# Kernel tuning notes

Measured on AMD Instinct MI355X. Metric: run time of the kernel, lower is better.

Reference implementation:

```python
import jax, jax.numpy as jnp
import numpy as np
import math

D_MODEL = 1024
NUM_HEADS = 16
D_K = D_MODEL // NUM_HEADS
NUM_BUCKETS = 32
MAX_DISTANCE = 512  # PositionalEncoding max_len


def _relative_position_bucket(relative_position):
    # Faithful to the torch code: both signs add num_buckets//2 (==16), rp==0 adds 0.
    half = NUM_BUCKETS // 2            # 16
    max_exact = NUM_BUCKETS // 4       # 8
    base = (relative_position > 0).astype(jnp.int32) * half \
         + (relative_position < 0).astype(jnp.int32) * half
    arp = jnp.abs(relative_position)
    is_small = arp < max_exact
    safe = jnp.maximum(arp, 1).astype(jnp.float32)  # avoid log(0); masked by is_small anyway
    large = max_exact + (jnp.log(safe / max_exact)
                         / math.log(MAX_DISTANCE / max_exact)
                         * (half - max_exact)).astype(jnp.int32)  # trunc == torch .long()
    large = jnp.minimum(large, half - 1)
    return base + jnp.where(is_small, arp, large)


def compute_bias(rel_bias_table, seq_length):
    ctx = jnp.arange(seq_length, dtype=jnp.int32)[:, None]
    mem = jnp.arange(seq_length, dtype=jnp.int32)[None, :]
    buckets = _relative_position_bucket(mem - ctx)        # [S, S]
    values = rel_bias_table[buckets]                       # [S, S, H]
    return jnp.transpose(values, (2, 0, 1))[None]          # [1, H, S, S]


def setup_inputs() -> dict:
    key = jax.random.key(0)
    ks = jax.random.split(key, 12)
    B, S, D = 2, 2048, D_MODEL
    scale = 1.0 / math.sqrt(D)
    inp = {
        "query": jax.random.normal(ks[0], (B, S, D), jnp.float32),
        "key": jax.random.normal(ks[1], (B, S, D), jnp.float32),
        "value": jax.random.normal(ks[2], (B, S, D), jnp.float32),
        "Wq": jax.random.normal(ks[3], (D, D), jnp.float32) * scale,
        "bq": jnp.zeros((D,), jnp.float32),
        "Wk": jax.random.normal(ks[4], (D, D), jnp.float32) * scale,
        "bk": jnp.zeros((D,), jnp.float32),
        "Wv": jax.random.normal(ks[5], (D, D), jnp.float32) * scale,
        "bv": jnp.zeros((D,), jnp.float32),
        "Wo": jax.random.normal(ks[6], (D, D), jnp.float32) * scale,
        "bo": jnp.zeros((D,), jnp.float32),
        "rel_bias_table": jax.random.normal(ks[7], (NUM_BUCKETS, NUM_HEADS), jnp.float32) * 0.1,
    }
    return inp


def reference(query, key, value, Wq, bq, Wk, bk, Wv, bv, Wo, bo, rel_bias_table):
    B, Sq, D = query.shape
    Sk = key.shape[1]
    H, dk = NUM_HEADS, D_K
    q = (query @ Wq + bq).reshape(B, Sq, H, dk)
    k = (key @ Wk + bk).reshape(B, Sk, H, dk)
    v = (value @ Wv + bv).reshape(B, Sk, H, dk)
    scores = jnp.einsum('bqhd,bkhd->bhqk', q, k) / math.sqrt(dk)  # [B,H,Sq,Sk]
    position_bias = compute_bias(rel_bias_table, max(Sq, Sk))[:, :, :Sq, :Sk]
    scores = scores + position_bias  # broadcast over batch (torch expand)
    attn_weights = jax.nn.softmax(scores, axis=-1)
    # dropout is identity in eval / p=0
    context = jnp.einsum('bhqk,bkhd->bqhd', attn_weights, v).reshape(B, Sq, D)
    output = context @ Wo + bo
    pb = jnp.broadcast_to(position_bias, (B, H, Sq, Sk))
    return output, attn_weights, pb
```

## Files before the change

### kernel.cpp

```cpp
#include <hip/hip_runtime.h>
#include <hip/hip_bf16.h>

#define BN 2
#define SEQ 2048
#define DM 1024
#define NH 16
#define DK 64

using f32x4  = __attribute__((ext_vector_type(4))) float;
using bf16x8 = __attribute__((ext_vector_type(8))) __bf16;
using short8 = __attribute__((ext_vector_type(8))) short;

static_assert(sizeof(bf16x8) == 16, "bf16x8 must be 16B");

#define MFMA16(a, b, c) __builtin_amdgcn_mfma_f32_16x16x32_bf16(a, b, c, 0, 0, 0)

__device__ __forceinline__ unsigned short f2b(float f) {
    __hip_bfloat16 h = __float2bfloat16(f);
    return __builtin_bit_cast(unsigned short, h);
}

__device__ __forceinline__ bf16x8 load_bf8(const unsigned short* p) {
    short8 s = *reinterpret_cast<const short8*>(p);
    return __builtin_bit_cast(bf16x8, s);
}

__global__ void bias_table_kernel(const float* __restrict__ rel,
                                  float* __restrict__ bias_val) {
    int idx = blockIdx.x * 256 + threadIdx.x;
    if (idx >= NH * 4095) return;
    int h = idx / 4095;
    int dd = idx - h * 4095;
    int d = dd - 2047;
    int a = d < 0 ? -d : d;
    int bucket;
    if (a == 0) bucket = 0;
    else if (a < 8) bucket = 16 + a;
    else {
        int k = (a >= 14) + (a >= 23) + (a >= 39) + (a >= 64) +
                (a >= 108) + (a >= 182) + (a >= 305);
        bucket = 24 + k;
    }
    bias_val[h * 4095 + dd] = rel[bucket * NH + h];
}

__global__ __launch_bounds__(256) void wtrans_kernel(
        const float* __restrict__ W0, const float* __restrict__ W1,
        const float* __restrict__ W2, const float* __restrict__ W3,
        unsigned short* __restrict__ T0, unsigned short* __restrict__ T1,
        unsigned short* __restrict__ T2, unsigned short* __restrict__ T3) {
    constexpr int P = 68;
    __shared__ unsigned short lt[64 * P];
    const int mz = blockIdx.z;
    const float* W = mz == 0 ? W0 : mz == 1 ? W1 : mz == 2 ? W2 : W3;
    unsigned short* T = mz == 0 ? T0 : mz == 1 ? T1 : mz == 2 ? T2 : T3;
    const int k0 = blockIdx.x * 64, n0 = blockIdx.y * 64;
    const int tid = threadIdx.x;
#pragma unroll
    for (int p = 0; p < 4; ++p) {
        int r = p * 16 + (tid >> 4);
        int c = (tid & 15) * 4;
        float4 vv = *(const float4*)&W[(size_t)(k0 + r) * DM + n0 + c];
#pragma unroll
        for (int j = 0; j < 4; ++j) {
            int n = c + j;
            float x = j == 0 ? vv.x : j == 1 ? vv.y : j == 2 ? vv.z : vv.w;
            lt[n * P + (r ^ ((n & 7) << 3))] = f2b(x);
        }
    }
    __syncthreads();
#pragma unroll
    for (int p = 0; p < 2; ++p) {
        int rn = p * 32 + (tid >> 3);
        int ck = (tid & 7) * 8;
        int ckx = ck ^ ((rn & 7) << 3);
        ushort4 a0 = *(ushort4*)&lt[rn * P + ckx];
        ushort4 a1 = *(ushort4*)&lt[rn * P + ckx + 4];
        *(ushort4*)&T[(size_t)(n0 + rn) * DM + k0 + ck] = a0;
        *(ushort4*)&T[(size_t)(n0 + rn) * DM + k0 + ck + 4] = a1;
    }
}

__global__ __launch_bounds__(256) void qkv_gemm(
        const float* __restrict__ Aq, const float* __restrict__ Ak, const float* __restrict__ Av,
        const unsigned short* __restrict__ Wtq, const unsigned short* __restrict__ Wtk,
        const unsigned short* __restrict__ Wtv,
        const float* __restrict__ bq, const float* __restrict__ bk, const float* __restrict__ bv,
        unsigned short* __restrict__ Qp, unsigned short* __restrict__ Kh,
        unsigned short* __restrict__ Vt) {
    constexpr int KP = 40;
    __shared__ unsigned short la[128 * KP];
    __shared__ unsigned short lb[128 * KP];
    const int mat = blockIdx.z;
    const float* A = mat == 0 ? Aq : mat == 1 ? Ak : Av;
    const unsigned short* Wt = mat == 0 ? Wtq : mat == 1 ? Wtk : Wtv;
    const float* bias = mat == 0 ? bq : mat == 1 ? bk : bv;
    const float outscale = mat == 0 ? 0.125f : 1.0f;
    const int tid = threadIdx.x;
    const int m0 = blockIdx.y * 128, n0 = blockIdx.x * 128;
    const int lane = tid & 63, wid = tid >> 6;
    const int wm0 = (wid >> 1) * 64, wn0 = (wid & 1) * 64;
    const int l15 = lane & 15, l4 = lane >> 4;
    f32x4 acc[4][4] = {};

    for (int kt = 0; kt < 32; ++kt) {
        const int k0 = kt * 32;
#pragma unroll
        for (int i = 0; i < 4; ++i) {
            int idx = tid + i * 256;
            int row = idx >> 3, c4 = (idx & 7) * 4;
            float4 v = *(const float4*)(A + (size_t)(m0 + row) * DM + k0 + c4);
            ushort4 u; u.x = f2b(v.x); u.y = f2b(v.y); u.z = f2b(v.z); u.w = f2b(v.w);
            *(ushort4*)&la[row * KP + c4] = u;
        }
#pragma unroll
        for (int i = 0; i < 2; ++i) {
            int idx = tid + i * 256;
            int row = idx >> 2, c8 = (idx & 3) * 8;
            *(int4*)&lb[row * KP + c8] =
                *(const int4*)&Wt[(size_t)(n0 + row) * DM + k0 + c8];
        }
        __syncthreads();
        bf16x8 af[4], bfv[4];
#pragma unroll
        for (int m = 0; m < 4; ++m)
            af[m] = load_bf8(&la[(wm0 + m * 16 + l15) * KP + l4 * 8]);
#pragma unroll
        for (int n = 0; n < 4; ++n)
            bfv[n] = load_bf8(&lb[(wn0 + n * 16 + l15) * KP + l4 * 8]);
#pragma unroll
        for (int m = 0; m < 4; ++m)
#pragma unroll
            for (int n = 0; n < 4; ++n)
                acc[m][n] = MFMA16(af[m], bfv[n], acc[m][n]);
        __syncthreads();
    }

    float bv4[4];
#pragma unroll
    for (int n = 0; n < 4; ++n) bv4[n] = bias[n0 + wn0 + n * 16 + l15];
#pragma unroll
    for (int m = 0; m < 4; ++m) {
#pragma unroll
        for (int n = 0; n < 4; ++n) {
            int gcol = n0 + wn0 + n * 16 + l15;
#pragma unroll
            for (int r = 0; r < 4; ++r) {
                int grow = m0 + wm0 + m * 16 + l4 * 4 + r;
                float val = (acc[m][n][r] + bv4[n]) * outscale;
                unsigned short ob = f2b(val);
                int b = grow >> 11, s = grow & 2047;
                int hh = gcol >> 6, dl = gcol & 63;
                if (mat == 0) {
                    Qp[(size_t)grow * DM + gcol] = ob;
                } else if (mat == 1) {
                    Kh[(((size_t)(b * NH + hh) * SEQ + s) << 6) + dl] = ob;
                } else {
                    Vt[(((size_t)(b * NH + hh) * DK + dl) << 11) + s] = ob;
                }
            }
        }
    }
}

__global__ __launch_bounds__(256) void o_gemm(
        const unsigned short* __restrict__ Actx, const unsigned short* __restrict__ Wto,
        const float* __restrict__ bo, float* __restrict__ out) {
    constexpr int KP = 40;
    __shared__ unsigned short la[64 * KP];
    __shared__ unsigned short lb[128 * KP];
    const int tid = threadIdx.x;
    const int m0 = blockIdx.y * 64, n0 = blockIdx.x * 128;
    const int lane = tid & 63, wid = tid >> 6;
    const int wm0 = (wid >> 1) * 32, wn0 = (wid & 1) * 64;
    const int l15 = lane & 15, l4 = lane >> 4;
    f32x4 acc[2][4] = {};

    for (int kt = 0; kt < 32; ++kt) {
        const int k0 = kt * 32;
        {
            int row = tid >> 2, c8 = (tid & 3) * 8;
            *(int4*)&la[row * KP + c8] =
                *(const int4*)&Actx[(size_t)(m0 + row) * DM + k0 + c8];
        }
#pragma unroll
        for (int i = 0; i < 2; ++i) {
            int idx = tid + i * 256;
            int row = idx >> 2, c8 = (idx & 3) * 8;
            *(int4*)&lb[row * KP + c8] =
                *(const int4*)&Wto[(size_t)(n0 + row) * DM + k0 + c8];
        }
        __syncthreads();
        bf16x8 af[2], bfv[4];
#pragma unroll
        for (int m = 0; m < 2; ++m)
            af[m] = load_bf8(&la[(wm0 + m * 16 + l15) * KP + l4 * 8]);
#pragma unroll
        for (int n = 0; n < 4; ++n)
            bfv[n] = load_bf8(&lb[(wn0 + n * 16 + l15) * KP + l4 * 8]);
#pragma unroll
        for (int m = 0; m < 2; ++m)
#pragma unroll
            for (int n = 0; n < 4; ++n)
                acc[m][n] = MFMA16(af[m], bfv[n], acc[m][n]);
        __syncthreads();
    }

#pragma unroll
    for (int m = 0; m < 2; ++m)
#pragma unroll
        for (int n = 0; n < 4; ++n) {
            int gcol = n0 + wn0 + n * 16 + l15;
            float bb = bo[gcol];
#pragma unroll
            for (int r = 0; r < 4; ++r) {
                int grow = m0 + wm0 + m * 16 + l4 * 4 + r;
                out[(size_t)grow * DM + gcol] = acc[m][n][r] + bb;
            }
        }
}

__global__ __launch_bounds__(256, 4) void attn5_kernel(
        const unsigned short* __restrict__ Qp, const unsigned short* __restrict__ Kh,
        const unsigned short* __restrict__ Vt, const float* __restrict__ bias_val,
        float* __restrict__ attn_out, float* __restrict__ pb_out,
        unsigned short* __restrict__ ctx) {
    __shared__ float bias_lds[2112];
    __shared__ float wtile[2][4][16 * 36];
    const int tid = threadIdx.x;
    const int lane = tid & 63, wid = tid >> 6;
    const int l15 = lane & 15, l4 = lane >> 4;
    const int bid = (blockIdx.x & 7) * 128 + (blockIdx.x >> 3);
    const int qb = bid & 31;
    const int h = (bid >> 5) & 15;
    const int b = bid >> 9;
    const int q0 = qb * 64;
    const int qw = q0 + wid * 16;

    {
        const float* bp = bias_val + h * 4095 + (2047 - (q0 + 63));
        for (int i = tid; i < 2111; i += 256) bias_lds[i] = bp[i];
    }
    __syncthreads();

    const unsigned short* qbase = Qp + (size_t)(b * SEQ + qw + l15) * DM + h * DK;
    bf16x8 qa0 = load_bf8(qbase + l4 * 8);
    bf16x8 qa1 = load_bf8(qbase + 32 + l4 * 8);

    const unsigned short* kbase = Kh + (((size_t)(b * NH + h) * SEQ) << 6);
    const int bbase = 63 - wid * 16 - l4 * 4;

    float m[4], l[4];
#pragma unroll
    for (int r = 0; r < 4; ++r) { m[r] = -3e38f; l[r] = 0.f; }

    for (int c0 = 0; c0 < SEQ; c0 += 32) {
        const unsigned short* kp = kbase + ((size_t)(c0 + l15) << 6);
        bf16x8 k00 = load_bf8(kp + l4 * 8);
        bf16x8 k01 = load_bf8(kp + 32 + l4 * 8);
        bf16x8 k10 = load_bf8(kp + (16 << 6) + l4 * 8);
        bf16x8 k11 = load_bf8(kp + (16 << 6) + 32 + l4 * 8);
        f32x4 a0 = {}, a1 = {};
        a0 = MFMA16(qa0, k00, a0); a0 = MFMA16(qa1, k01, a0);
        a1 = MFMA16(qa0, k10, a1); a1 = MFMA16(qa1, k11, a1);
#pragma unroll
        for (int r = 0; r < 4; ++r) {
            float s0 = a0[r] + bias_lds[c0 + l15 + bbase - r];
            float s1 = a1[r] + bias_lds[c0 + 16 + l15 + bbase - r];
            float cm = fmaxf(s0, s1);
            if (cm > m[r]) { l[r] *= __expf(m[r] - cm); m[r] = cm; }
            l[r] += __expf(s0 - m[r]) + __expf(s1 - m[r]);
        }
    }
#pragma unroll
    for (int off = 1; off < 16; off <<= 1) {
#pragma unroll
        for (int r = 0; r < 4; ++r) {
            float om = __shfl_xor(m[r], off);
            float ol = __shfl_xor(l[r], off);
            float M = fmaxf(m[r], om);
            l[r] = l[r] * __expf(m[r] - M) + ol * __expf(om - M);
            m[r] = M;
        }
    }
    float invl[4];
#pragma unroll
    for (int r = 0; r < 4; ++r) invl[r] = 1.0f / l[r];

    float* abase = attn_out + ((size_t)((b * NH + h) * SEQ + qw)) * SEQ;
    float* pbase = pb_out + ((size_t)((b * NH + h) * SEQ + qw)) * SEQ;
    const unsigned short* vbase = Vt + (((size_t)(b * NH + h) * DK) << 11);
    f32x4 cacc[4] = {};

    bf16x8 k00, k01, k10, k11;
    {
        const unsigned short* kp = kbase + ((size_t)l15 << 6);
        k00 = load_bf8(kp + l4 * 8);
        k01 = load_bf8(kp + 32 + l4 * 8);
        k10 = load_bf8(kp + (16 << 6) + l4 * 8);
        k11 = load_bf8(kp + (16 << 6) + 32 + l4 * 8);
    }
    const int srow = lane >> 2, scg = (lane & 3) * 8;
    int cur = 0;
    for (int c0 = 0; c0 < SEQ; c0 += 32, cur ^= 1) {
        f32x4 a0 = {}, a1 = {};
        a0 = MFMA16(qa0, k00, a0); a0 = MFMA16(qa1, k01, a0);
        a1 = MFMA16(qa0, k10, a1); a1 = MFMA16(qa1, k11, a1);
        const int cn = (c0 + 32) & (SEQ - 1);
        const unsigned short* kp = kbase + ((size_t)(cn + l15) << 6);
        k00 = load_bf8(kp + l4 * 8);
        k01 = load_bf8(kp + 32 + l4 * 8);
        k10 = load_bf8(kp + (16 << 6) + l4 * 8);
        k11 = load_bf8(kp + (16 << 6) + 32 + l4 * 8);
        bf16x8 vv0 = load_bf8(vbase + ((size_t)(0 * 16 + l15) << 11) + c0 + l4 * 8);
        bf16x8 vv1 = load_bf8(vbase + ((size_t)(1 * 16 + l15) << 11) + c0 + l4 * 8);
        bf16x8 vv2 = load_bf8(vbase + ((size_t)(2 * 16 + l15) << 11) + c0 + l4 * 8);
        bf16x8 vv3 = load_bf8(vbase + ((size_t)(3 * 16 + l15) << 11) + c0 + l4 * 8);
        float* wt = wtile[cur][wid];
#pragma unroll
        for (int r = 0; r < 4; ++r) {
            int row = l4 * 4 + r;
            float w0 = __expf(a0[r] + bias_lds[c0 + l15 + bbase - r] - m[r]) * invl[r];
            float w1 = __expf(a1[r] + bias_lds[c0 + 16 + l15 + bbase - r] - m[r]) * invl[r];
            wt[row * 36 + l15] = w0;
            wt[row * 36 + 16 + l15] = w1;
        }
        asm volatile("s_waitcnt lgkmcnt(0)" ::: "memory");
        __builtin_amdgcn_sched_barrier(0);
        {
            float4 v0 = *(const float4*)&wt[srow * 36 + scg];
            float4 v1 = *(const float4*)&wt[srow * 36 + scg + 4];
            float* gp = abase + (size_t)srow * SEQ + c0 + scg;
            *(float4*)gp = v0;
            *(float4*)(gp + 4) = v1;
        }
        {
            const int ib = c0 + scg + bbase + l4 * 4 - srow;
            float4 p0, p1;
            p0.x = bias_lds[ib + 0]; p0.y = bias_lds[ib + 1];
            p0.z = bias_lds[ib + 2]; p0.w = bias_lds[ib + 3];
            p1.x = bias_lds[ib + 4]; p1.y = bias_lds[ib + 5];
            p1.z = bias_lds[ib + 6]; p1.w = bias_lds[ib + 7];
            float* gp = pbase + (size_t)srow * SEQ + c0 + scg;
            *(float4*)gp = p0;
            *(float4*)(gp + 4) = p1;
        }
        float4 pA = *(const float4*)&wt[l15 * 36 + l4 * 8];
        float4 pB = *(const float4*)&wt[l15 * 36 + l4 * 8 + 4];
        short8 ps;
        ps[0] = (short)f2b(pA.x); ps[1] = (short)f2b(pA.y);
        ps[2] = (short)f2b(pA.z); ps[3] = (short)f2b(pA.w);
        ps[4] = (short)f2b(pB.x); ps[5] = (short)f2b(pB.y);
        ps[6] = (short)f2b(pB.z); ps[7] = (short)f2b(pB.w);
        bf16x8 pf = __builtin_bit_cast(bf16x8, ps);
        cacc[0] = MFMA16(pf, vv0, cacc[0]);
        cacc[1] = MFMA16(pf, vv1, cacc[1]);
        cacc[2] = MFMA16(pf, vv2, cacc[2]);
        cacc[3] = MFMA16(pf, vv3, cacc[3]);
    }
#pragma unroll
    for (int d0 = 0; d0 < 4; ++d0)
#pragma unroll
        for (int r = 0; r < 4; ++r)
            ctx[(size_t)(b * SEQ + qw + l4 * 4 + r) * DM + h * DK + d0 * 16 + l15] =
                f2b(cacc[d0][r]);
}

extern "C" void kernel_launch(void* const* d_in, const int* in_sizes, int n_in,
                              void* d_out, int out_size, void* d_ws, size_t ws_size,
                              hipStream_t stream) {
    const float* query = (const float*)d_in[0];
    const float* key   = (const float*)d_in[1];
    const float* value = (const float*)d_in[2];
    const float* Wq = (const float*)d_in[3];
    const float* bq = (const float*)d_in[4];
    const float* Wk = (const float*)d_in[5];
    const float* bk = (const float*)d_in[6];
    const float* Wv = (const float*)d_in[7];
    const float* bv = (const float*)d_in[8];
    const float* Wo = (const float*)d_in[9];
    const float* bo = (const float*)d_in[10];
    const float* rel = (const float*)d_in[11];

    float* out = (float*)d_out;
    float* attn_out = out + (size_t)BN * SEQ * DM;
    float* pb_out = attn_out + (size_t)BN * NH * SEQ * SEQ;

    char* ws = (char*)d_ws;
    float* bias_val = (float*)ws;
    unsigned short* Qp  = (unsigned short*)(ws + 262144);
    unsigned short* Kh  = Qp + (size_t)BN * SEQ * DM;
    unsigned short* Vt  = Kh + (size_t)BN * SEQ * DM;
    unsigned short* ctx = Vt + (size_t)BN * SEQ * DM;
    unsigned short* Wtq = ctx + (size_t)BN * SEQ * DM;
    unsigned short* Wtk = Wtq + (size_t)DM * DM;
    unsigned short* Wtv = Wtk + (size_t)DM * DM;
    unsigned short* Wto = Wtv + (size_t)DM * DM;

    bias_table_kernel<<<256, 256, 0, stream>>>(rel, bias_val);
    wtrans_kernel<<<dim3(16, 16, 4), 256, 0, stream>>>(Wq, Wk, Wv, Wo, Wtq, Wtk, Wtv, Wto);
    qkv_gemm<<<dim3(8, 32, 3), 256, 0, stream>>>(query, key, value, Wtq, Wtk, Wtv,
                                                 bq, bk, bv, Qp, Kh, Vt);
    attn5_kernel<<<BN * NH * (SEQ / 64), 256, 0, stream>>>(Qp, Kh, Vt, bias_val,
                                                           attn_out, pb_out, ctx);
    o_gemm<<<dim3(8, 64), 256, 0, stream>>>(ctx, Wto, bo, out);
}
```

Measured before the change: 592.8 us.

## Replace online softmax max with Cauchy-Schwarz bound and log-sum-exp normalization

Result: slower. 647.2 us (+9.2%).

```diff
diff --git a/kernel.cpp b/kernel.cpp
--- a/kernel.cpp
+++ b/kernel.cpp
@@ -87,7 +87,8 @@
         const unsigned short* __restrict__ Wtv,
         const float* __restrict__ bq, const float* __restrict__ bk, const float* __restrict__ bv,
         unsigned short* __restrict__ Qp, unsigned short* __restrict__ Kh,
-        unsigned short* __restrict__ Vt) {
+        unsigned short* __restrict__ Vt,
+        float* __restrict__ qnorm, float* __restrict__ khpart) {
     constexpr int KP = 40;
     __shared__ unsigned short la[128 * KP];
     __shared__ unsigned short lb[128 * KP];
@@ -139,6 +140,12 @@
     float bv4[4];
 #pragma unroll
     for (int n = 0; n < 4; ++n) bv4[n] = bias[n0 + wn0 + n * 16 + l15];
+    float nsq[4][4];
+#pragma unroll
+    for (int m = 0; m < 4; ++m)
+#pragma unroll
+        for (int r = 0; r < 4; ++r) nsq[m][r] = 0.f;
+
 #pragma unroll
     for (int m = 0; m < 4; ++m) {
 #pragma unroll
@@ -148,6 +155,7 @@
             for (int r = 0; r < 4; ++r) {
                 int grow = m0 + wm0 + m * 16 + l4 * 4 + r;
                 float val = (acc[m][n][r] + bv4[n]) * outscale;
+                if (mat < 2) nsq[m][r] += val * val;
                 unsigned short ob = f2b(val);
                 int b = grow >> 11, s = grow & 2047;
                 int hh = gcol >> 6, dl = gcol & 63;
@@ -159,6 +167,43 @@
                     Vt[(((size_t)(b * NH + hh) * DK + dl) << 11) + s] = ob;
                 }
             }
+        }
+    }
+
+    if (mat < 2) {
+        const int hh = (n0 + wn0) >> 6;
+        const int bh = ((m0 + wm0) >> 11) * NH + hh;
+#pragma unroll
+        for (int m = 0; m < 4; ++m)
+#pragma unroll
+            for (int r = 0; r < 4; ++r) {
+                float s2 = nsq[m][r];
+                s2 += __shfl_xor(s2, 1);
+                s2 += __shfl_xor(s2, 2);
+                s2 += __shfl_xor(s2, 4);
+                s2 += __shfl_xor(s2, 8);
+                nsq[m][r] = s2;
+            }
+        if (mat == 0) {
+            if (l15 == 0) {
+#pragma unroll
+                for (int m = 0; m < 4; ++m)
+#pragma unroll
+                    for (int r = 0; r < 4; ++r) {
+                        int grow = m0 + wm0 + m * 16 + l4 * 4 + r;
+                        qnorm[bh * SEQ + (grow & 2047)] = sqrtf(nsq[m][r]);
+                    }
+            }
+        } else {
+            float rmax = 0.f;
+#pragma unroll
+            for (int m = 0; m < 4; ++m)
+#pragma unroll
+                for (int r = 0; r < 4; ++r) rmax = fmaxf(rmax, nsq[m][r]);
+            rmax = fmaxf(rmax, __shfl_xor(rmax, 16));
+            rmax = fmaxf(rmax, __shfl_xor(rmax, 32));
+            if (lane == 0)
+                khpart[bh * 32 + (((m0 + wm0) & 2047) >> 6)] = sqrtf(rmax);
         }
     }
 }
@@ -220,13 +265,15 @@
         }
 }
 
-__global__ __launch_bounds__(256, 4) void attn5_kernel(
+__global__ __launch_bounds__(256, 4) void attn6_kernel(
         const unsigned short* __restrict__ Qp, const unsigned short* __restrict__ Kh,
         const unsigned short* __restrict__ Vt, const float* __restrict__ bias_val,
+        const float* __restrict__ qnorm, const float* __restrict__ khpart,
         float* __restrict__ attn_out, float* __restrict__ pb_out,
         unsigned short* __restrict__ ctx) {
     __shared__ float bias_lds[2112];
     __shared__ float wtile[2][4][16 * 36];
+    __shared__ float redmax[4];
     const int tid = threadIdx.x;
     const int lane = tid & 63, wid = tid >> 6;
     const int l15 = lane & 15, l4 = lane >> 4;
@@ -236,62 +283,46 @@
     const int b = bid >> 9;
     const int q0 = qb * 64;
     const int qw = q0 + wid * 16;
-
+    const int bh = b * NH + h;
+
+    float pmax = -1e30f;
     {
         const float* bp = bias_val + h * 4095 + (2047 - (q0 + 63));
-        for (int i = tid; i < 2111; i += 256) bias_lds[i] = bp[i];
-    }
+        for (int i = tid; i < 2111; i += 256) {
+            float x = bp[i];
+            bias_lds[i] = x;
+            pmax = fmaxf(pmax, x);
+        }
+    }
+#pragma unroll
+    for (int off = 1; off < 64; off <<= 1) pmax = fmaxf(pmax, __shfl_xor(pmax, off));
+    if (lane == 0) redmax[wid] = pmax;
     __syncthreads();
+    const float bmax = fmaxf(fmaxf(redmax[0], redmax[1]), fmaxf(redmax[2], redmax[3]));
+
+    float khv = (lane < 32) ? khpart[bh * 32 + lane] : 0.f;
+#pragma unroll
+    for (int off = 1; off < 64; off <<= 1) khv = fmaxf(khv, __shfl_xor(khv, off));
+
+    float Mr[4];
+#pragma unroll
+    for (int r = 0; r < 4; ++r)
+        Mr[r] = qnorm[bh * SEQ + qw + l4 * 4 + r] * 1.01f * khv + bmax + 0.1f;
 
     const unsigned short* qbase = Qp + (size_t)(b * SEQ + qw + l15) * DM + h * DK;
     bf16x8 qa0 = load_bf8(qbase + l4 * 8);
     bf16x8 qa1 = load_bf8(qbase + 32 + l4 * 8);
 
-    const unsigned short* kbase = Kh + (((size_t)(b * NH + h) * SEQ) << 6);
+    const unsigned short* kbase = Kh + (((size_t)bh * SEQ) << 6);
+    const unsigned short* vbase = Vt + (((size_t)bh * DK) << 11);
     const int bbase = 63 - wid * 16 - l4 * 4;
-
-    float m[4], l[4];
-#pragma unroll
-    for (int r = 0; r < 4; ++r) { m[r] = -3e38f; l[r] = 0.f; }
-
-    for (int c0 = 0; c0 < SEQ; c0 += 32) {
-        const unsigned short* kp = kbase + ((size_t)(c0 + l15) << 6);
-        bf16x8 k00 = load_bf8(kp + l4 * 8);
-        bf16x8 k01 = load_bf8(kp + 32 + l4 * 8);
-        bf16x8 k10 = load_bf8(kp + (16 << 6) + l4 * 8);
-        bf16x8 k11 = load_bf8(kp + (16 << 6) + 32 + l4 * 8);
-        f32x4 a0 = {}, a1 = {};
-        a0 = MFMA16(qa0, k00, a0); a0 = MFMA16(qa1, k01, a0);
-        a1 = MFMA16(qa0, k10, a1); a1 = MFMA16(qa1, k11, a1);
-#pragma unroll
-        for (int r = 0; r < 4; ++r) {
-            float s0 = a0[r] + bias_lds[c0 + l15 + bbase - r];
-            float s1 = a1[r] + bias_lds[c0 + 16 + l15 + bbase - r];
-            float cm = fmaxf(s0, s1);
-            if (cm > m[r]) { l[r] *= __expf(m[r] - cm); m[r] = cm; }
-            l[r] += __expf(s0 - m[r]) + __expf(s1 - m[r]);
-        }
-    }
-#pragma unroll
-    for (int off = 1; off < 16; off <<= 1) {
-#pragma unroll
-        for (int r = 0; r < 4; ++r) {
-            float om = __shfl_xor(m[r], off);
-            float ol = __shfl_xor(l[r], off);
-            float M = fmaxf(m[r], om);
-            l[r] = l[r] * __expf(m[r] - M) + ol * __expf(om - M);
-            m[r] = M;
-        }
-    }
-    float invl[4];
-#pragma unroll
-    for (int r = 0; r < 4; ++r) invl[r] = 1.0f / l[r];
-
-    float* abase = attn_out + ((size_t)((b * NH + h) * SEQ + qw)) * SEQ;
-    float* pbase = pb_out + ((size_t)((b * NH + h) * SEQ + qw)) * SEQ;
-    const unsigned short* vbase = Vt + (((size_t)(b * NH + h) * DK) << 11);
-    f32x4 cacc[4] = {};
-
+    const int srow = lane >> 2, scg = (lane & 3) * 8;
+    const int bb2 = 63 - wid * 16;
+
+    float* pbase = pb_out + ((size_t)(bh * SEQ + qw)) * SEQ;
+    float* abase = attn_out + ((size_t)(bh * SEQ + qw)) * SEQ;
+
+    float lsum[4] = {0.f, 0.f, 0.f, 0.f};
     bf16x8 k00, k01, k10, k11;
     {
         const unsigned short* kp = kbase + ((size_t)l15 << 6);
@@ -300,9 +331,7 @@
         k10 = load_bf8(kp + (16 << 6) + l4 * 8);
         k11 = load_bf8(kp + (16 << 6) + 32 + l4 * 8);
     }
-    const int srow = lane >> 2, scg = (lane & 3) * 8;
-    int cur = 0;
-    for (int c0 = 0; c0 < SEQ; c0 += 32, cur ^= 1) {
+    for (int c0 = 0; c0 < SEQ; c0 += 32) {
         f32x4 a0 = {}, a1 = {};
         a0 = MFMA16(qa0, k00, a0); a0 = MFMA16(qa1, k01, a0);
         a1 = MFMA16(qa0, k10, a1); a1 = MFMA16(qa1, k11, a1);
@@ -312,16 +341,69 @@
         k01 = load_bf8(kp + 32 + l4 * 8);
         k10 = load_bf8(kp + (16 << 6) + l4 * 8);
         k11 = load_bf8(kp + (16 << 6) + 32 + l4 * 8);
-        bf16x8 vv0 = load_bf8(vbase + ((size_t)(0 * 16 + l15) << 11) + c0 + l4 * 8);
-        bf16x8 vv1 = load_bf8(vbase + ((size_t)(1 * 16 + l15) << 11) + c0 + l4 * 8);
-        bf16x8 vv2 = load_bf8(vbase + ((size_t)(2 * 16 + l15) << 11) + c0 + l4 * 8);
-        bf16x8 vv3 = load_bf8(vbase + ((size_t)(3 * 16 + l15) << 11) + c0 + l4 * 8);
+        {
+            const int ib = c0 + scg + bb2 - srow;
+            float4 p0, p1;
+            p0.x = bias_lds[ib + 0]; p0.y = bias_lds[ib + 1];
+            p0.z = bias_lds[ib + 2]; p0.w = bias_lds[ib + 3];
+            p1.x = bias_lds[ib + 4]; p1.y = bias_lds[ib + 5];
+            p1.z = bias_lds[ib + 6]; p1.w = bias_lds[ib + 7];
+            float* gp = pbase + (size_t)srow * SEQ + c0 + scg;
+            *(float4*)gp = p0;
+            *(float4*)(gp + 4) = p1;
+        }
+#pragma unroll
+        for (int r = 0; r < 4; ++r) {
+            float e0 = __expf(a0[r] + bias_lds[c0 + l15 + bbase - r] - Mr[r]);
+            float e1 = __expf(a1[r] + bias_lds[c0 + 16 + l15 + bbase - r] - Mr[r]);
+            lsum[r] += e0 + e1;
+        }
+    }
+    float Mlog[4];
+#pragma unroll
+    for (int r = 0; r < 4; ++r) {
+        float s = lsum[r];
+        s += __shfl_xor(s, 1);
+        s += __shfl_xor(s, 2);
+        s += __shfl_xor(s, 4);
+        s += __shfl_xor(s, 8);
+        Mlog[r] = Mr[r] + __logf(s);
+    }
+
+    f32x4 cacc[4] = {};
+    bf16x8 vv0, vv1, vv2, vv3;
+    {
+        const unsigned short* kp = kbase + ((size_t)l15 << 6);
+        k00 = load_bf8(kp + l4 * 8);
+        k01 = load_bf8(kp + 32 + l4 * 8);
+        k10 = load_bf8(kp + (16 << 6) + l4 * 8);
+        k11 = load_bf8(kp + (16 << 6) + 32 + l4 * 8);
+        vv0 = load_bf8(vbase + ((size_t)(0 * 16 + l15) << 11) + l4 * 8);
+        vv1 = load_bf8(vbase + ((size_t)(1 * 16 + l15) << 11) + l4 * 8);
+        vv2 = load_bf8(vbase + ((size_t)(2 * 16 + l15) << 11) + l4 * 8);
+        vv3 = load_bf8(vbase + ((size_t)(3 * 16 + l15) << 11) + l4 * 8);
+    }
+    int cur = 0;
+    for (int c0 = 0; c0 < SEQ; c0 += 32, cur ^= 1) {
+        f32x4 a0 = {}, a1 = {};
+        a0 = MFMA16(qa0, k00, a0); a0 = MFMA16(qa1, k01, a0);
+        a1 = MFMA16(qa0, k10, a1); a1 = MFMA16(qa1, k11, a1);
+        const int cn = (c0 + 32) & (SEQ - 1);
+        const unsigned short* kp = kbase + ((size_t)(cn + l15) << 6);
+        bf16x8 kn00 = load_bf8(kp + l4 * 8);
+        bf16x8 kn01 = load_bf8(kp + 32 + l4 * 8);
+        bf16x8 kn10 = load_bf8(kp + (16 << 6) + l4 * 8);
+        bf16x8 kn11 = load_bf8(kp + (16 << 6) + 32 + l4 * 8);
+        bf16x8 vn0 = load_bf8(vbase + ((size_t)(0 * 16 + l15) << 11) + cn + l4 * 8);
+        bf16x8 vn1 = load_bf8(vbase + ((size_t)(1 * 16 + l15) << 11) + cn + l4 * 8);
+        bf16x8 vn2 = load_bf8(vbase + ((size_t)(2 * 16 + l15) << 11) + cn + l4 * 8);
+        bf16x8 vn3 = load_bf8(vbase + ((size_t)(3 * 16 + l15) << 11) + cn + l4 * 8);
         float* wt = wtile[cur][wid];
 #pragma unroll
         for (int r = 0; r < 4; ++r) {
             int row = l4 * 4 + r;
-            float w0 = __expf(a0[r] + bias_lds[c0 + l15 + bbase - r] - m[r]) * invl[r];
-            float w1 = __expf(a1[r] + bias_lds[c0 + 16 + l15 + bbase - r] - m[r]) * invl[r];
+            float w0 = __expf(a0[r] + bias_lds[c0 + l15 + bbase - r] - Mlog[r]);
+            float w1 = __expf(a1[r] + bias_lds[c0 + 16 + l15 + bbase - r] - Mlog[r]);
             wt[row * 36 + l15] = w0;
             wt[row * 36 + 16 + l15] = w1;
         }
@@ -333,17 +415,6 @@
             float* gp = abase + (size_t)srow * SEQ + c0 + scg;
             *(float4*)gp = v0;
             *(float4*)(gp + 4) = v1;
-        }
-        {
-            const int ib = c0 + scg + bbase + l4 * 4 - srow;
-            float4 p0, p1;
-            p0.x = bias_lds[ib + 0]; p0.y = bias_lds[ib + 1];
-            p0.z = bias_lds[ib + 2]; p0.w = bias_lds[ib + 3];
-            p1.x = bias_lds[ib + 4]; p1.y = bias_lds[ib + 5];
-            p1.z = bias_lds[ib + 6]; p1.w = bias_lds[ib + 7];
-            float* gp = pbase + (size_t)srow * SEQ + c0 + scg;
-            *(float4*)gp = p0;
-            *(float4*)(gp + 4) = p1;
         }
         float4 pA = *(const float4*)&wt[l15 * 36 + l4 * 8];
         float4 pB = *(const float4*)&wt[l15 * 36 + l4 * 8 + 4];
@@ -357,6 +428,8 @@
         cacc[1] = MFMA16(pf, vv1, cacc[1]);
         cacc[2] = MFMA16(pf, vv2, cacc[2]);
         cacc[3] = MFMA16(pf, vv3, cacc[3]);
+        k00 = kn00; k01 = kn01; k10 = kn10; k11 = kn11;
+        vv0 = vn0; vv1 = vn1; vv2 = vn2; vv3 = vn3;
     }
 #pragma unroll
     for (int d0 = 0; d0 < 4; ++d0)
@@ -396,12 +469,15 @@
     unsigned short* Wtk = Wtq + (size_t)DM * DM;
     unsigned short* Wtv = Wtk + (size_t)DM * DM;
     unsigned short* Wto = Wtv + (size_t)DM * DM;
+    float* qnorm = (float*)(Wto + (size_t)DM * DM);
+    float* khpart = qnorm + (size_t)BN * NH * SEQ;
 
     bias_table_kernel<<<256, 256, 0, stream>>>(rel, bias_val);
     wtrans_kernel<<<dim3(16, 16, 4), 256, 0, stream>>>(Wq, Wk, Wv, Wo, Wtq, Wtk, Wtv, Wto);
     qkv_gemm<<<dim3(8, 32, 3), 256, 0, stream>>>(query, key, value, Wtq, Wtk, Wtv,
-                                                 bq, bk, bv, Qp, Kh, Vt);
-    attn5_kernel<<<BN * NH * (SEQ / 64), 256, 0, stream>>>(Qp, Kh, Vt, bias_val,
+                                                 bq, bk, bv, Qp, Kh, Vt, qnorm, khpart);
+    attn6_kernel<<<BN * NH * (SEQ / 64), 256, 0, stream>>>(Qp, Kh, Vt, bias_val,
+                                                           qnorm, khpart,
                                                            attn_out, pb_out, ctx);
     o_gemm<<<dim3(8, 64), 256, 0, stream>>>(ctx, Wto, bo, out);
 }
```
